# Kernel tuning notes

Measured on AMD Instinct MI355X. Metric: run time of the kernel, lower is better.

Reference implementation:

```python
import jax, jax.numpy as jnp
import numpy as np

L, I, H = 4, 256, 512          # layers, input_size, hidden_size
SH, LH, GH = 4, 2, 2            # short/long/global heads
NH, HD, FF = SH + LH + GH, H // (SH + LH + GH), 2 * H
S, B = 1024, 8                  # seq (AST nodes), batch
EPS = 1e-5
NEG = -1e9


def _ln(x, g, b):
    m = jnp.mean(x, axis=-1, keepdims=True)
    v = jnp.var(x, axis=-1, keepdims=True)
    return (x - m) * jax.lax.rsqrt(v + EPS) * g + b


def setup_inputs() -> dict:
    key = jax.random.key(0)
    ks = jax.random.split(key, 10)
    w = lambda k, shape: jax.random.normal(k, shape, jnp.float32) * 0.02
    return {
        "nodes": jax.random.normal(ks[0], (S, B, I), jnp.float32),
        "dist": jax.random.randint(ks[1], (B, S, S), 0, 5, jnp.int32),
        "dense_w": w(ks[2], (H, I)), "dense_b": jnp.zeros((H,), jnp.float32),
        "dense_ln_g": jnp.ones((H,), jnp.float32), "dense_ln_b": jnp.zeros((H,), jnp.float32),
        "qkv_w": w(ks[3], (L, 3 * H, H)), "qkv_b": jnp.zeros((L, 3 * H), jnp.float32),
        "out_w": w(ks[4], (L, H, H)), "out_b": jnp.zeros((L, H), jnp.float32),
        "ln1_g": jnp.ones((L, H), jnp.float32), "ln1_b": jnp.zeros((L, H), jnp.float32),
        "ffn_w1": w(ks[5], (L, FF, H)), "ffn_b1": jnp.zeros((L, FF), jnp.float32),
        "ffn_w2": w(ks[6], (L, H, FF)), "ffn_b2": jnp.zeros((L, H), jnp.float32),
        "ln2_g": jnp.ones((L, H), jnp.float32), "ln2_b": jnp.zeros((L, H), jnp.float32),
        "bn_g": jnp.ones((H,), jnp.float32), "bn_b": jnp.zeros((H,), jnp.float32),
    }


def _mask_bias(dist):
    # dist: [B,S,S] int -> additive bias [B,NH,S,S]
    short = (dist == 1)[:, None]                       # [B,1,S,S]
    longm = (dist >= 1)[:, None]
    globm = jnp.broadcast_to((dist[:, 0:1, :] >= 1)[:, None], (dist.shape[0], 1, S, S))
    allowed = jnp.concatenate([
        jnp.broadcast_to(short, (dist.shape[0], SH, S, S)),
        jnp.broadcast_to(longm, (dist.shape[0], LH, S, S)),
        jnp.broadcast_to(globm, (dist.shape[0], GH, S, S)),
    ], axis=1)
    allowed = allowed | jnp.eye(S, dtype=bool)
    return jnp.where(allowed, 0.0, NEG).astype(jnp.float32)


def _forward(nodes, dist, dense_w, dense_b, dense_ln_g, dense_ln_b,
             qkv_w, qkv_b, out_w, out_b, ln1_g, ln1_b,
             ffn_w1, ffn_b1, ffn_w2, ffn_b2, ln2_g, ln2_b, bn_g, bn_b):
    x = jnp.transpose(nodes, (1, 0, 2))                # [B,S,I]
    x = _ln(x @ dense_w.T + dense_b, dense_ln_g, dense_ln_b)  # [B,S,H]
    bias = _mask_bias(dist)                            # [B,NH,S,S]
    scale = 1.0 / np.sqrt(HD)

    def layer(x, p):
        (wqkv, bqkv, wo, bo, g1, b1, w1, bf1, w2, bf2, g2, b2) = p
        qkv = x @ wqkv.T + bqkv                        # [B,S,3H]
        q, k, v = jnp.split(qkv, 3, axis=-1)
        q = q.reshape(B, S, NH, HD).transpose(0, 2, 1, 3)
        k = k.reshape(B, S, NH, HD).transpose(0, 2, 1, 3)
        v = v.reshape(B, S, NH, HD).transpose(0, 2, 1, 3)
        scores = jnp.einsum('bhqd,bhkd->bhqk', q, k) * scale + bias
        attn = jax.nn.softmax(scores, axis=-1)
        o = jnp.einsum('bhqk,bhkd->bhqd', attn, v)
        o = o.transpose(0, 2, 1, 3).reshape(B, S, H) @ wo.T + bo
        x = _ln(x + o, g1, b1)
        f = jax.nn.relu(x @ w1.T + bf1) @ w2.T + bf2
        x = _ln(x + f, g2, b2)
        return x, None

    params = (qkv_w, qkv_b, out_w, out_b, ln1_g, ln1_b,
              ffn_w1, ffn_b1, ffn_w2, ffn_b2, ln2_g, ln2_b)
    x, _ = jax.lax.scan(layer, x, params)
    hidden = x[:, 0]                                   # first token -> [B,H]
    m = jnp.mean(hidden, axis=0)
    v = jnp.var(hidden, axis=0)
    return (hidden - m) * jax.lax.rsqrt(v + EPS) * bn_g + bn_b


def reference(nodes, dist, dense_w, dense_b, dense_ln_g, dense_ln_b,
              qkv_w, qkv_b, out_w, out_b, ln1_g, ln1_b,
              ffn_w1, ffn_b1, ffn_w2, ffn_b2, ln2_g, ln2_b, bn_g, bn_b):
    return _forward(nodes, dist, dense_w, dense_b, dense_ln_g, dense_ln_b,
                    qkv_w, qkv_b, out_w, out_b, ln1_g, ln1_b,
                    ffn_w1, ffn_b1, ffn_w2, ffn_b2, ln2_g, ln2_b, bn_g, bn_b)
```

## Files before the change

kernel.cpp:

```cpp
#include <hip/hip_runtime.h>
#include <hip/hip_bf16.h>
#include <math.h>

#define LAYERS 4
#define IDIM 256
#define HDIM 512
#define NH 8
#define HD 64
#define FF 1024
#define SEQ 1024
#define BATCH 8
#define EPS 1e-5f

typedef __attribute__((ext_vector_type(8))) short short8;
typedef __attribute__((ext_vector_type(4))) short short4v;
typedef __attribute__((ext_vector_type(4))) float f32x4;
typedef __attribute__((ext_vector_type(4))) int int4v;
typedef __attribute__((ext_vector_type(2))) unsigned int uint2v;
typedef unsigned long long u64;

__device__ __forceinline__ short f2bf(float f) {
    unsigned u = __float_as_uint(f);
    u = (u + 0x7FFFu + ((u >> 16) & 1u)) >> 16;
    return (short)u;
}
__device__ __forceinline__ float bf2f(short s) {
    return __uint_as_float(((unsigned)(unsigned short)s) << 16);
}
__device__ __forceinline__ void gll16(const void* g, void* l) {
    __builtin_amdgcn_global_load_lds(
        (const __attribute__((address_space(1))) unsigned int*)g,
        (__attribute__((address_space(3))) unsigned int*)l, 16, 0, 0);
}

#define CVT_P0 131072u
#define CVT_P1 3276800u
#define CVT_P2 4325376u
#define CVT_P3 6422528u
#define CVT_TOT 8519680u
__global__ __launch_bounds__(256) void cvt_all(const float* __restrict__ s0, short* __restrict__ d0,
                                               const float* __restrict__ s1, short* __restrict__ d1,
                                               const float* __restrict__ s2, short* __restrict__ d2,
                                               const float* __restrict__ s3, short* __restrict__ d3,
                                               const float* __restrict__ s4, short* __restrict__ d4) {
    size_t i = ((size_t)blockIdx.x * 256 + threadIdx.x) * 4;
    const float* s; short* d; size_t off;
    if (i < CVT_P0)      { s = s0; d = d0; off = i; }
    else if (i < CVT_P1) { s = s1; d = d1; off = i - CVT_P0; }
    else if (i < CVT_P2) { s = s2; d = d2; off = i - CVT_P1; }
    else if (i < CVT_P3) { s = s3; d = d3; off = i - CVT_P2; }
    else                 { s = s4; d = d4; off = i - CVT_P3; }
    f32x4 f = *(const f32x4*)(s + off);
    short4v o = {f2bf(f[0]), f2bf(f[1]), f2bf(f[2]), f2bf(f[3])};
    *(short4v*)(d + off) = o;
}

__global__ __launch_bounds__(256) void transpose_nodes(const float* __restrict__ nodes,
                                                       short* __restrict__ xt) {
    size_t idx = ((size_t)blockIdx.x * 256 + threadIdx.x) * 4;
    int i  = idx & (IDIM - 1);
    int sb = idx >> 8;
    int b  = sb & (BATCH - 1);
    int s  = sb >> 3;
    f32x4 f = *(const f32x4*)(nodes + idx);
    short4v o = {f2bf(f[0]), f2bf(f[1]), f2bf(f[2]), f2bf(f[3])};
    *(short4v*)(xt + ((size_t)b * SEQ + s) * IDIM + i) = o;
}

__global__ __launch_bounds__(256) void build_masks(const int* __restrict__ dist,
                                                   u64* __restrict__ mS,
                                                   u64* __restrict__ mL,
                                                   u64* __restrict__ mG) {
    int t = blockIdx.x * 256 + threadIdx.x;
    int w = t & 15, q = (t >> 4) & 1023, b = t >> 14;
    const int4v* dp = (const int4v*)(dist + ((size_t)b * SEQ + q) * SEQ + w * 64);
    u64 bs = 0, bl = 0;
#pragma unroll
    for (int i = 0; i < 16; i++) {
        int4v d = dp[i];
#pragma unroll
        for (int j = 0; j < 4; j++) {
            bs |= (u64)(d[j] == 1) << (i * 4 + j);
            bl |= (u64)(d[j] >= 1) << (i * 4 + j);
        }
    }
    mS[((size_t)b * SEQ + q) * 16 + w] = bs;
    mL[((size_t)b * SEQ + q) * 16 + w] = bl;
    if (q == 0) mG[b * 16 + w] = bl;
}

template<int BM, int BK>
__global__ __launch_bounds__(256, 2)
void gemm_bf16(const short* __restrict__ A, const short* __restrict__ W,
               const float* __restrict__ bias, short* __restrict__ C,
               short* __restrict__ vt, int M, int N, int K, int relu) {
    constexpr int UPR = BK / 8;
    constexpr int RPC = 512 / BK;
    __shared__ __align__(16) short As[BM * BK];
    __shared__ __align__(16) short Ws[128 * BK];
    const int tid = threadIdx.x;
    const int w = tid >> 6, lane = tid & 63;
    const int l15 = lane & 15, quad = lane >> 4;
    const int m0 = blockIdx.y * BM, n0 = blockIdx.x * 128;

    constexpr int NI = (BM == 128) ? 4 : 2;
    const int wm = (BM == 128) ? (w >> 1) * 64 : 0;
    const int wn = (BM == 128) ? (w & 1) * 64 : w * 32;

    f32x4 acc[4][NI];
#pragma unroll
    for (int mi = 0; mi < 4; mi++)
#pragma unroll
        for (int ni = 0; ni < NI; ni++) acc[mi][ni] = (f32x4){0.f, 0.f, 0.f, 0.f};

    const int r_in = (BK == 64) ? (lane >> 3) : (lane >> 4);
    const int c8   = lane & (UPR - 1);

    for (int k0 = 0; k0 < K; k0 += BK) {
#pragma unroll
        for (int rep = 0; rep < BM * BK / 2048; rep++) {
            int chunk = rep * 4 + w;
            int row = chunk * RPC + r_in;
            const short* src = A + (size_t)(m0 + row) * K + k0 + ((c8 ^ (row & (UPR - 1))) << 3);
            gll16(src, (char*)As + chunk * 1024);
        }
#pragma unroll
        for (int rep = 0; rep < 128 * BK / 2048; rep++) {
            int chunk = rep * 4 + w;
            int row = chunk * RPC + r_in;
            const short* src = W + (size_t)(n0 + row) * K + k0 + ((c8 ^ (row & (UPR - 1))) << 3);
            gll16(src, (char*)Ws + chunk * 1024);
        }
        __syncthreads();
#pragma unroll
        for (int ks = 0; ks < BK / 32; ks++) {
            short8 af[4], wf[NI];
            const int dblk = ks * 4 + quad;
#pragma unroll
            for (int mi = 0; mi < 4; mi++) {
                int row = wm + mi * 16 + l15;
                af[mi] = *(const short8*)((const char*)As + row * (BK * 2) + ((dblk ^ (row & (UPR - 1))) << 4));
            }
#pragma unroll
            for (int ni = 0; ni < NI; ni++) {
                int row = wn + ni * 16 + l15;
                wf[ni] = *(const short8*)((const char*)Ws + row * (BK * 2) + ((dblk ^ (row & (UPR - 1))) << 4));
            }
#pragma unroll
            for (int mi = 0; mi < 4; mi++)
#pragma unroll
                for (int ni = 0; ni < NI; ni++)
                    acc[mi][ni] = __builtin_amdgcn_mfma_f32_16x16x32_bf16(
                        af[mi], wf[ni], acc[mi][ni], 0, 0, 0);
        }
        __syncthreads();
    }
    if (vt && n0 >= 1024) {
#pragma unroll
        for (int ni = 0; ni < NI; ni++) {
            int n = n0 + wn + ni * 16 + l15;
            int d = n - 1024, h = d >> 6, dd = d & 63;
            float bz = bias[n];
#pragma unroll
            for (int mi = 0; mi < 4; mi++) {
                int mbase = m0 + wm + mi * 16 + quad * 4;
                int b = mbase >> 10, s = mbase & 1023;
                int tile = s >> 6, j = (s & 63) >> 2;
                size_t off = ((size_t)(b * NH + h) * HD + dd) * SEQ
                           + tile * 64 + (j & 7) * 8 + (j >> 3) * 4;
                short4v pk;
#pragma unroll
                for (int r = 0; r < 4; r++) pk[r] = f2bf(acc[mi][ni][r] + bz);
                *(short4v*)(vt + off) = pk;
            }
        }
    } else {
#pragma unroll
        for (int ni = 0; ni < NI; ni++) {
            int n = n0 + wn + ni * 16 + l15;
            float bz = bias[n];
#pragma unroll
            for (int mi = 0; mi < 4; mi++) {
#pragma unroll
                for (int r = 0; r < 4; r++) {
                    int m = m0 + wm + mi * 16 + quad * 4 + r;
                    float v = acc[mi][ni][r] + bz;
                    if (relu) v = fmaxf(v, 0.f);
                    C[(size_t)m * N + n] = f2bf(v);
                }
            }
        }
    }
}

#define EXP2SC 0.18033688011112042f
__global__ __launch_bounds__(256, 4)
void attn_mfma(const short* __restrict__ qkv, const short* __restrict__ vt,
               const u64* __restrict__ maskS, const u64* __restrict__ maskL,
               const u64* __restrict__ maskG, short* __restrict__ out) {
    const int tid = threadIdx.x;
    const int w = tid >> 6, lane = tid & 63, l15 = lane & 15, quad = lane >> 4;
    const int p = blockIdx.x;
    const int g_ = (p & 7) + 8 * (p >> 7);
    const int qt = (p >> 3) & 15;
    const int b = g_ >> 3, h = g_ & 7;
    const int q = qt * 64 + w * 16 + l15;

    __shared__ __align__(16) short Ks[128 * 64];
    __shared__ __align__(16) short Vs[128 * 64];

    short8 qf[2];
    {
        const short* qrow = qkv + ((size_t)(b * SEQ + q) * 1536) + h * 64;
#pragma unroll
        for (int ks = 0; ks < 2; ks++)
            qf[ks] = *(const short8*)(qrow + ks * 32 + quad * 8);
    }
    const u64* mrow = (h < 4) ? (maskS + ((size_t)b * SEQ + q) * 16)
                   : (h < 6) ? (maskL + ((size_t)b * SEQ + q) * 16)
                   :           (maskG + (size_t)b * 16);

    f32x4 of[4];
#pragma unroll
    for (int mt = 0; mt < 4; mt++) of[mt] = (f32x4){0.f, 0.f, 0.f, 0.f};
    float lsum = 0.f;

    const int r_in = lane >> 3, c8 = lane & 7;
    const int swz = (c8 ^ r_in) << 3;
    const short* kp = qkv + ((size_t)b * SEQ + r_in) * 1536 + 512 + h * 64 + swz;
    const short* vp = vt + ((size_t)((b * NH + h) * HD) + r_in) * SEQ + swz;
    const int fsw = (l15 & 7);

    for (int kt = 0; kt < SEQ; kt += 128) {
#pragma unroll
        for (int rep = 0; rep < 4; rep++) {
            int c = rep * 4 + w;
            gll16(kp + (size_t)(kt + c * 8) * 1536, (char*)Ks + c * 1024);
        }
#pragma unroll
        for (int rep = 0; rep < 4; rep++) {
            int v = rep * 4 + w;
            gll16(vp + (size_t)((v & 7) * 8) * SEQ + kt + (v >> 3) * 64,
                  (char*)Vs + v * 1024);
        }
        __syncthreads();

#pragma unroll
        for (int t = 0; t < 2; t++) {
            f32x4 sa[4];
#pragma unroll
            for (int g = 0; g < 4; g++) sa[g] = (f32x4){0.f, 0.f, 0.f, 0.f};
#pragma unroll
            for (int ks = 0; ks < 2; ks++) {
                const int dblk = ks * 4 + quad;
#pragma unroll
                for (int g = 0; g < 4; g++) {
                    int row = t * 64 + g * 16 + l15;
                    short8 kf = *(const short8*)((const char*)Ks + row * 128 + ((dblk ^ fsw) << 4));
                    sa[g] = __builtin_amdgcn_mfma_f32_16x16x32_bf16(kf, qf[ks], sa[g], 0, 0, 0);
                }
            }
            u64 mw = mrow[(kt >> 6) + t];
            if ((q >> 6) == (kt >> 6) + t) mw |= 1ull << (q & 63);
            u64 mq = mw >> (quad * 4);
            unsigned mlo = (unsigned)mq, mhi = (unsigned)(mq >> 32);
            short4v pfrag[4];
#pragma unroll
            for (int g = 0; g < 4; g++) {
                unsigned mg = ((g & 2) ? mhi : mlo) >> ((g & 1) * 16);
                float pv[4];
#pragma unroll
                for (int r = 0; r < 4; r++) {
                    float bias = ((mg >> r) & 1u) ? 0.f : -1e9f;
                    pv[r] = exp2f(fmaf(sa[g][r], EXP2SC, bias));
                    lsum += pv[r];
                }
                uint2v pk;
                pk[0] = __builtin_amdgcn_perm(__float_as_uint(pv[1]), __float_as_uint(pv[0]), 0x07060302u);
                pk[1] = __builtin_amdgcn_perm(__float_as_uint(pv[3]), __float_as_uint(pv[2]), 0x07060302u);
                pfrag[g] = __builtin_bit_cast(short4v, pk);
            }
#pragma unroll
            for (int g01 = 0; g01 < 2; g01++) {
                const int u = g01 * 4 + quad;
#pragma unroll
                for (int mt = 0; mt < 4; mt++) {
                    int row = mt * 16 + l15;
                    short8 vv = *(const short8*)((const char*)Vs + t * 8192 + row * 128 + ((u ^ fsw) << 4));
                    short4v vlo = {vv[0], vv[1], vv[2], vv[3]};
                    short4v vhi = {vv[4], vv[5], vv[6], vv[7]};
                    of[mt] = __builtin_amdgcn_mfma_f32_16x16x16bf16_1k(vlo, pfrag[g01], of[mt], 0, 0, 0);
                    of[mt] = __builtin_amdgcn_mfma_f32_16x16x16bf16_1k(vhi, pfrag[g01 + 2], of[mt], 0, 0, 0);
                }
            }
        }
        __syncthreads();
    }
    lsum += __shfl_xor(lsum, 16);
    lsum += __shfl_xor(lsum, 32);
    float inv = 1.f / lsum;
#pragma unroll
    for (int mt = 0; mt < 4; mt++) {
        short4v pk;
#pragma unroll
        for (int r = 0; r < 4; r++) pk[r] = f2bf(of[mt][r] * inv);
        *(short4v*)(out + ((size_t)(b * SEQ + q) * HDIM) + h * 64 + mt * 16 + quad * 4) = pk;
    }
}

__global__ __launch_bounds__(256) void ln_bf16(const short* __restrict__ x,
                                               const short* __restrict__ r,
                                               const float* __restrict__ g,
                                               const float* __restrict__ b,
                                               short* __restrict__ y) {
    const int wv = threadIdx.x >> 6, lane = threadIdx.x & 63;
    const size_t row = (size_t)blockIdx.x * 4 + wv;
    const size_t base = row * HDIM + lane * 8;
    short8 xv = *(const short8*)(x + base);
    float v[8];
#pragma unroll
    for (int i = 0; i < 8; i++) v[i] = bf2f(xv[i]);
    if (r) {
        short8 rv = *(const short8*)(r + base);
#pragma unroll
        for (int i = 0; i < 8; i++) v[i] += bf2f(rv[i]);
    }
    float s = 0.f, ss = 0.f;
#pragma unroll
    for (int i = 0; i < 8; i++) { s += v[i]; ss += v[i] * v[i]; }
#pragma unroll
    for (int off = 1; off < 64; off <<= 1) {
        s  += __shfl_xor(s, off);
        ss += __shfl_xor(ss, off);
    }
    const float mean = s * (1.f / HDIM);
    const float var  = ss * (1.f / HDIM) - mean * mean;
    const float inv  = rsqrtf(var + EPS);
    f32x4 g0 = *(const f32x4*)(g + lane * 8), g1 = *(const f32x4*)(g + lane * 8 + 4);
    f32x4 b0 = *(const f32x4*)(b + lane * 8), b1 = *(const f32x4*)(b + lane * 8 + 4);
    short8 o;
#pragma unroll
    for (int i = 0; i < 4; i++) o[i]     = f2bf((v[i]     - mean) * inv * g0[i] + b0[i]);
#pragma unroll
    for (int i = 0; i < 4; i++) o[i + 4] = f2bf((v[i + 4] - mean) * inv * g1[i] + b1[i]);
    *(short8*)(y + base) = o;
}

__global__ __launch_bounds__(256) void final_bn(const short* __restrict__ X,
                                                const float* __restrict__ g,
                                                const float* __restrict__ bb,
                                                float* __restrict__ out) {
    int h = blockIdx.x * 256 + threadIdx.x;
    if (h >= HDIM) return;
    float vals[BATCH];
    float m = 0.f;
#pragma unroll
    for (int b = 0; b < BATCH; b++) {
        vals[b] = bf2f(X[(size_t)b * SEQ * HDIM + h]);
        m += vals[b];
    }
    m *= (1.f / BATCH);
    float v = 0.f;
#pragma unroll
    for (int b = 0; b < BATCH; b++) { float d = vals[b] - m; v += d * d; }
    v *= (1.f / BATCH);
    float inv = rsqrtf(v + EPS);
#pragma unroll
    for (int b = 0; b < BATCH; b++)
        out[b * HDIM + h] = (vals[b] - m) * inv * g[h] + bb[h];
}

extern "C" void kernel_launch(void* const* d_in, const int* in_sizes, int n_in,
                              void* d_out, int out_size, void* d_ws, size_t ws_size,
                              hipStream_t stream) {
    const float* nodes      = (const float*)d_in[0];
    const int*   dist       = (const int*)  d_in[1];
    const float* dense_w    = (const float*)d_in[2];
    const float* dense_b    = (const float*)d_in[3];
    const float* dense_ln_g = (const float*)d_in[4];
    const float* dense_ln_b = (const float*)d_in[5];
    const float* qkv_w      = (const float*)d_in[6];
    const float* qkv_b      = (const float*)d_in[7];
    const float* out_w      = (const float*)d_in[8];
    const float* out_b      = (const float*)d_in[9];
    const float* ln1_g      = (const float*)d_in[10];
    const float* ln1_b      = (const float*)d_in[11];
    const float* ffn_w1     = (const float*)d_in[12];
    const float* ffn_b1     = (const float*)d_in[13];
    const float* ffn_w2     = (const float*)d_in[14];
    const float* ffn_b2     = (const float*)d_in[15];
    const float* ln2_g      = (const float*)d_in[16];
    const float* ln2_b      = (const float*)d_in[17];
    const float* bn_g       = (const float*)d_in[18];
    const float* bn_b       = (const float*)d_in[19];
    float* out = (float*)d_out;

    const int M = BATCH * SEQ;
    const size_t MB = 1024 * 1024;
    char* ws = (char*)d_ws;
    short* Wd   = (short*)(ws + 0 * MB);
    short* Wqkv = (short*)(ws + 1 * MB);
    short* Wo   = (short*)(ws + 9 * MB);
    short* W1   = (short*)(ws + 13 * MB);
    short* W2   = (short*)(ws + 18 * MB);
    u64*   mS   = (u64*)(ws + 23 * MB);
    u64*   mL   = (u64*)(ws + 24 * MB);
    u64*   mG   = (u64*)(ws + 25 * MB);
    short* X    = (short*)(ws + 26 * MB);
    short* QKV  = (short*)(ws + 34 * MB);
    short* Vt   = (short*)(ws + 58 * MB);
    short* AT   = (short*)(ws + 66 * MB);
    short* O2   = (short*)(ws + 74 * MB);
    short* XT   = QKV;
    short* F1   = QKV;
    short* F2   = AT;

    cvt_all<<<CVT_TOT / 1024, 256, 0, stream>>>(dense_w, Wd, qkv_w, Wqkv,
                                                out_w, Wo, ffn_w1, W1, ffn_w2, W2);
    transpose_nodes<<<(SEQ * BATCH * IDIM) / 1024, 256, 0, stream>>>(nodes, XT);
    build_masks<<<(BATCH * SEQ * 16) / 256, 256, 0, stream>>>(dist, mS, mL, mG);

    gemm_bf16<64, 128><<<dim3(HDIM / 128, M / 64), 256, 0, stream>>>(
        XT, Wd, dense_b, O2, nullptr, M, HDIM, IDIM, 0);
    ln_bf16<<<M / 4, 256, 0, stream>>>(O2, nullptr, dense_ln_g, dense_ln_b, X);

    for (int l = 0; l < LAYERS; l++) {
        const short* wqkv = Wqkv + (size_t)l * 3 * HDIM * HDIM;
        const float* bqkv = qkv_b + (size_t)l * 3 * HDIM;
        const short* wo   = Wo + (size_t)l * HDIM * HDIM;
        const float* bo   = out_b + (size_t)l * HDIM;
        const short* w1   = W1 + (size_t)l * FF * HDIM;
        const float* b1   = ffn_b1 + (size_t)l * FF;
        const short* w2   = W2 + (size_t)l * HDIM * FF;
        const float* b2   = ffn_b2 + (size_t)l * HDIM;

        gemm_bf16<128, 64><<<dim3(3 * HDIM / 128, M / 128), 256, 0, stream>>>(
            X, wqkv, bqkv, QKV, Vt, M, 3 * HDIM, HDIM, 0);
        attn_mfma<<<1024, 256, 0, stream>>>(QKV, Vt, mS, mL, mG, AT);
        gemm_bf16<64, 128><<<dim3(HDIM / 128, M / 64), 256, 0, stream>>>(
            AT, wo, bo, O2, nullptr, M, HDIM, HDIM, 0);
        ln_bf16<<<M / 4, 256, 0, stream>>>(X, O2, ln1_g + l * HDIM, ln1_b + l * HDIM, X);
        gemm_bf16<128, 64><<<dim3(FF / 128, M / 128), 256, 0, stream>>>(
            X, w1, b1, F1, nullptr, M, FF, HDIM, 1);
        gemm_bf16<64, 128><<<dim3(HDIM / 128, M / 64), 256, 0, stream>>>(
            F1, w2, b2, F2, nullptr, M, HDIM, FF, 0);
        ln_bf16<<<M / 4, 256, 0, stream>>>(X, F2, ln2_g + l * HDIM, ln2_b + l * HDIM, X);
    }
    final_bn<<<(HDIM + 255) / 256, 256, 0, stream>>>(X, bn_g, bn_b, out);
}
```

Measured before the change: 643.3 us.

## Double-buffer GEMM shared-memory tiles and switch all GEMMs to 64x64 tiles

Adds ping-pong LDS buffers to the bf16 GEMM so the next K-slab's async global-to-LDS loads are issued before computing the current slab, dropping one barrier per iteration. All GEMM launches switch to BM=64, BK=64 tiles, which gives more blocks for the M=8192 problem, and launch bounds are raised to 3 blocks per CU. The change trades smaller per-block reuse for more parallelism and load/compute overlap, and the doubled LDS and tighter register budget may limit occupancy.

```diff
diff --git a/kernel.cpp b/kernel.cpp
--- a/kernel.cpp
+++ b/kernel.cpp
@@ -90,14 +90,16 @@
 }
 
 template<int BM, int BK>
-__global__ __launch_bounds__(256, 2)
+__global__ __launch_bounds__(256, 3)
 void gemm_bf16(const short* __restrict__ A, const short* __restrict__ W,
                const float* __restrict__ bias, short* __restrict__ C,
                short* __restrict__ vt, int M, int N, int K, int relu) {
     constexpr int UPR = BK / 8;
-    constexpr int RPC = 512 / BK;
-    __shared__ __align__(16) short As[BM * BK];
-    __shared__ __align__(16) short Ws[128 * BK];
+    constexpr int RPC = 1024 / (BK * 2);
+    constexpr int ACH = BM * BK * 2 / 1024;
+    constexpr int WCH = 128 * BK * 2 / 1024;
+    __shared__ __align__(16) short As[2][BM * BK];
+    __shared__ __align__(16) short Ws[2][128 * BK];
     const int tid = threadIdx.x;
     const int w = tid >> 6, lane = tid & 63;
     const int l15 = lane & 15, quad = lane >> 4;
@@ -113,25 +115,33 @@
 #pragma unroll
         for (int ni = 0; ni < NI; ni++) acc[mi][ni] = (f32x4){0.f, 0.f, 0.f, 0.f};
 
-    const int r_in = (BK == 64) ? (lane >> 3) : (lane >> 4);
-    const int c8   = lane & (UPR - 1);
-
-    for (int k0 = 0; k0 < K; k0 += BK) {
-#pragma unroll
-        for (int rep = 0; rep < BM * BK / 2048; rep++) {
+    const int r_in = lane / UPR;
+    const int c8   = lane % UPR;
+
+    auto stage = [&](int buf, int k0) {
+#pragma unroll
+        for (int rep = 0; rep < ACH / 4; rep++) {
             int chunk = rep * 4 + w;
             int row = chunk * RPC + r_in;
-            const short* src = A + (size_t)(m0 + row) * K + k0 + ((c8 ^ (row & (UPR - 1))) << 3);
-            gll16(src, (char*)As + chunk * 1024);
-        }
-#pragma unroll
-        for (int rep = 0; rep < 128 * BK / 2048; rep++) {
+            gll16(A + (size_t)(m0 + row) * K + k0 + ((c8 ^ (row & (UPR - 1))) << 3),
+                  (char*)As[buf] + chunk * 1024);
+        }
+#pragma unroll
+        for (int rep = 0; rep < WCH / 4; rep++) {
             int chunk = rep * 4 + w;
             int row = chunk * RPC + r_in;
-            const short* src = W + (size_t)(n0 + row) * K + k0 + ((c8 ^ (row & (UPR - 1))) << 3);
-            gll16(src, (char*)Ws + chunk * 1024);
-        }
+            gll16(W + (size_t)(n0 + row) * K + k0 + ((c8 ^ (row & (UPR - 1))) << 3),
+                  (char*)Ws[buf] + chunk * 1024);
+        }
+    };
+
+    stage(0, 0);
+    const int NIT = K / BK;
+    for (int it = 0; it < NIT; it++) {
         __syncthreads();
+        if (it + 1 < NIT) stage((it + 1) & 1, (it + 1) * BK);
+        const char* Ab = (const char*)As[it & 1];
+        const char* Wb = (const char*)Ws[it & 1];
 #pragma unroll
         for (int ks = 0; ks < BK / 32; ks++) {
             short8 af[4], wf[NI];
@@ -139,12 +149,12 @@
 #pragma unroll
             for (int mi = 0; mi < 4; mi++) {
                 int row = wm + mi * 16 + l15;
-                af[mi] = *(const short8*)((const char*)As + row * (BK * 2) + ((dblk ^ (row & (UPR - 1))) << 4));
+                af[mi] = *(const short8*)(Ab + row * (BK * 2) + ((dblk ^ (row & (UPR - 1))) << 4));
             }
 #pragma unroll
             for (int ni = 0; ni < NI; ni++) {
                 int row = wn + ni * 16 + l15;
-                wf[ni] = *(const short8*)((const char*)Ws + row * (BK * 2) + ((dblk ^ (row & (UPR - 1))) << 4));
+                wf[ni] = *(const short8*)(Wb + row * (BK * 2) + ((dblk ^ (row & (UPR - 1))) << 4));
             }
 #pragma unroll
             for (int mi = 0; mi < 4; mi++)
@@ -153,7 +163,6 @@
                     acc[mi][ni] = __builtin_amdgcn_mfma_f32_16x16x32_bf16(
                         af[mi], wf[ni], acc[mi][ni], 0, 0, 0);
         }
-        __syncthreads();
     }
     if (vt && n0 >= 1024) {
 #pragma unroll
@@ -420,7 +429,7 @@
     transpose_nodes<<<(SEQ * BATCH * IDIM) / 1024, 256, 0, stream>>>(nodes, XT);
     build_masks<<<(BATCH * SEQ * 16) / 256, 256, 0, stream>>>(dist, mS, mL, mG);
 
-    gemm_bf16<64, 128><<<dim3(HDIM / 128, M / 64), 256, 0, stream>>>(
+    gemm_bf16<64, 64><<<dim3(HDIM / 128, M / 64), 256, 0, stream>>>(
         XT, Wd, dense_b, O2, nullptr, M, HDIM, IDIM, 0);
     ln_bf16<<<M / 4, 256, 0, stream>>>(O2, nullptr, dense_ln_g, dense_ln_b, X);
 
@@ -434,15 +443,15 @@
         const short* w2   = W2 + (size_t)l * HDIM * FF;
         const float* b2   = ffn_b2 + (size_t)l * HDIM;
 
-        gemm_bf16<128, 64><<<dim3(3 * HDIM / 128, M / 128), 256, 0, stream>>>(
+        gemm_bf16<64, 64><<<dim3(3 * HDIM / 128, M / 64), 256, 0, stream>>>(
             X, wqkv, bqkv, QKV, Vt, M, 3 * HDIM, HDIM, 0);
         attn_mfma<<<1024, 256, 0, stream>>>(QKV, Vt, mS, mL, mG, AT);
-        gemm_bf16<64, 128><<<dim3(HDIM / 128, M / 64), 256, 0, stream>>>(
+        gemm_bf16<64, 64><<<dim3(HDIM / 128, M / 64), 256, 0, stream>>>(
             AT, wo, bo, O2, nullptr, M, HDIM, HDIM, 0);
         ln_bf16<<<M / 4, 256, 0, stream>>>(X, O2, ln1_g + l * HDIM, ln1_b + l * HDIM, X);
-        gemm_bf16<128, 64><<<dim3(FF / 128, M / 128), 256, 0, stream>>>(
+        gemm_bf16<64, 64><<<dim3(FF / 128, M / 64), 256, 0, stream>>>(
             X, w1, b1, F1, nullptr, M, FF, HDIM, 1);
-        gemm_bf16<64, 128><<<dim3(HDIM / 128, M / 64), 256, 0, stream>>>(
+        gemm_bf16<64, 64><<<dim3(HDIM / 128, M / 64), 256, 0, stream>>>(
             F1, w2, b2, F2, nullptr, M, HDIM, FF, 0);
         ln_bf16<<<M / 4, 256, 0, stream>>>(X, F2, ln2_g + l * HDIM, ln2_b + l * HDIM, X);
     }
```

Result: no change. 654.7 us (+1.8%).

## Use 16x16x32 MFMA for PV, permute K rows, fuse prep kernels

Applied to the files above, without the earlier changes.

Merges the three preprocessing kernels (weight conversion, node transpose, mask build) into one launch to cut launch overhead. In attention, the K tile is loaded with a permuted row order so that each lane's score fragment lines up with a contiguous 8-key chunk. That lets P·V use a single 16x16x32 bf16 MFMA per V read instead of two 16x16x16 ops, and V is now written in plain key order. The mask is applied by zeroing exp values instead of adding a -1e9 bias, using the hardware exp2 builtin. The row sum is split into two accumulators. The scheme relies on the K permutation, mask bit shifts and V layout staying consistent.

```diff
diff --git a/kernel.cpp b/kernel.cpp
--- a/kernel.cpp
+++ b/kernel.cpp
@@ -16,7 +16,7 @@
 typedef __attribute__((ext_vector_type(4))) short short4v;
 typedef __attribute__((ext_vector_type(4))) float f32x4;
 typedef __attribute__((ext_vector_type(4))) int int4v;
-typedef __attribute__((ext_vector_type(2))) unsigned int uint2v;
+typedef __attribute__((ext_vector_type(4))) unsigned int uint4v;
 typedef unsigned long long u64;
 
 __device__ __forceinline__ short f2bf(float f) {
@@ -31,6 +31,13 @@
     __builtin_amdgcn_global_load_lds(
         (const __attribute__((address_space(1))) unsigned int*)g,
         (__attribute__((address_space(3))) unsigned int*)l, 16, 0, 0);
+}
+__device__ __forceinline__ float fexp2(float x) {
+#if __has_builtin(__builtin_amdgcn_exp2f)
+    return __builtin_amdgcn_exp2f(x);
+#else
+    return exp2f(x);
+#endif
 }
 
 #define CVT_P0 131072u
@@ -38,55 +45,54 @@
 #define CVT_P2 4325376u
 #define CVT_P3 6422528u
 #define CVT_TOT 8519680u
-__global__ __launch_bounds__(256) void cvt_all(const float* __restrict__ s0, short* __restrict__ d0,
-                                               const float* __restrict__ s1, short* __restrict__ d1,
-                                               const float* __restrict__ s2, short* __restrict__ d2,
-                                               const float* __restrict__ s3, short* __restrict__ d3,
-                                               const float* __restrict__ s4, short* __restrict__ d4) {
-    size_t i = ((size_t)blockIdx.x * 256 + threadIdx.x) * 4;
-    const float* s; short* d; size_t off;
-    if (i < CVT_P0)      { s = s0; d = d0; off = i; }
-    else if (i < CVT_P1) { s = s1; d = d1; off = i - CVT_P0; }
-    else if (i < CVT_P2) { s = s2; d = d2; off = i - CVT_P1; }
-    else if (i < CVT_P3) { s = s3; d = d3; off = i - CVT_P2; }
-    else                 { s = s4; d = d4; off = i - CVT_P3; }
-    f32x4 f = *(const f32x4*)(s + off);
-    short4v o = {f2bf(f[0]), f2bf(f[1]), f2bf(f[2]), f2bf(f[3])};
-    *(short4v*)(d + off) = o;
-}
-
-__global__ __launch_bounds__(256) void transpose_nodes(const float* __restrict__ nodes,
-                                                       short* __restrict__ xt) {
-    size_t idx = ((size_t)blockIdx.x * 256 + threadIdx.x) * 4;
-    int i  = idx & (IDIM - 1);
-    int sb = idx >> 8;
-    int b  = sb & (BATCH - 1);
-    int s  = sb >> 3;
-    f32x4 f = *(const f32x4*)(nodes + idx);
-    short4v o = {f2bf(f[0]), f2bf(f[1]), f2bf(f[2]), f2bf(f[3])};
-    *(short4v*)(xt + ((size_t)b * SEQ + s) * IDIM + i) = o;
-}
-
-__global__ __launch_bounds__(256) void build_masks(const int* __restrict__ dist,
-                                                   u64* __restrict__ mS,
-                                                   u64* __restrict__ mL,
-                                                   u64* __restrict__ mG) {
-    int t = blockIdx.x * 256 + threadIdx.x;
-    int w = t & 15, q = (t >> 4) & 1023, b = t >> 14;
-    const int4v* dp = (const int4v*)(dist + ((size_t)b * SEQ + q) * SEQ + w * 64);
-    u64 bs = 0, bl = 0;
-#pragma unroll
-    for (int i = 0; i < 16; i++) {
-        int4v d = dp[i];
-#pragma unroll
-        for (int j = 0; j < 4; j++) {
-            bs |= (u64)(d[j] == 1) << (i * 4 + j);
-            bl |= (u64)(d[j] >= 1) << (i * 4 + j);
-        }
-    }
-    mS[((size_t)b * SEQ + q) * 16 + w] = bs;
-    mL[((size_t)b * SEQ + q) * 16 + w] = bl;
-    if (q == 0) mG[b * 16 + w] = bl;
+__global__ __launch_bounds__(256) void prep_all(
+    const float* __restrict__ s0, short* __restrict__ d0,
+    const float* __restrict__ s1, short* __restrict__ d1,
+    const float* __restrict__ s2, short* __restrict__ d2,
+    const float* __restrict__ s3, short* __restrict__ d3,
+    const float* __restrict__ s4, short* __restrict__ d4,
+    const float* __restrict__ nodes, short* __restrict__ xt,
+    const int* __restrict__ dist, u64* __restrict__ mS,
+    u64* __restrict__ mL, u64* __restrict__ mG) {
+    int blk = blockIdx.x;
+    if (blk < 8320) {
+        size_t i = ((size_t)blk * 256 + threadIdx.x) * 4;
+        const float* s; short* d; size_t off;
+        if (i < CVT_P0)      { s = s0; d = d0; off = i; }
+        else if (i < CVT_P1) { s = s1; d = d1; off = i - CVT_P0; }
+        else if (i < CVT_P2) { s = s2; d = d2; off = i - CVT_P1; }
+        else if (i < CVT_P3) { s = s3; d = d3; off = i - CVT_P2; }
+        else                 { s = s4; d = d4; off = i - CVT_P3; }
+        f32x4 f = *(const f32x4*)(s + off);
+        short4v o = {f2bf(f[0]), f2bf(f[1]), f2bf(f[2]), f2bf(f[3])};
+        *(short4v*)(d + off) = o;
+    } else if (blk < 8320 + 2048) {
+        size_t idx = ((size_t)(blk - 8320) * 256 + threadIdx.x) * 4;
+        int i  = idx & (IDIM - 1);
+        int sb = idx >> 8;
+        int b  = sb & (BATCH - 1);
+        int s  = sb >> 3;
+        f32x4 f = *(const f32x4*)(nodes + idx);
+        short4v o = {f2bf(f[0]), f2bf(f[1]), f2bf(f[2]), f2bf(f[3])};
+        *(short4v*)(xt + ((size_t)b * SEQ + s) * IDIM + i) = o;
+    } else {
+        int t = (blk - 10368) * 256 + threadIdx.x;
+        int w = t & 15, q = (t >> 4) & 1023, b = t >> 14;
+        const int4v* dp = (const int4v*)(dist + ((size_t)b * SEQ + q) * SEQ + w * 64);
+        u64 bs = 0, bl = 0;
+#pragma unroll
+        for (int i = 0; i < 16; i++) {
+            int4v d = dp[i];
+#pragma unroll
+            for (int j = 0; j < 4; j++) {
+                bs |= (u64)(d[j] == 1) << (i * 4 + j);
+                bl |= (u64)(d[j] >= 1) << (i * 4 + j);
+            }
+        }
+        mS[((size_t)b * SEQ + q) * 16 + w] = bs;
+        mL[((size_t)b * SEQ + q) * 16 + w] = bl;
+        if (q == 0) mG[b * 16 + w] = bl;
+    }
 }
 
 template<int BM, int BK>
@@ -165,9 +171,7 @@
             for (int mi = 0; mi < 4; mi++) {
                 int mbase = m0 + wm + mi * 16 + quad * 4;
                 int b = mbase >> 10, s = mbase & 1023;
-                int tile = s >> 6, j = (s & 63) >> 2;
-                size_t off = ((size_t)(b * NH + h) * HD + dd) * SEQ
-                           + tile * 64 + (j & 7) * 8 + (j >> 3) * 4;
+                size_t off = ((size_t)(b * NH + h) * HD + dd) * SEQ + s;
                 short4v pk;
 #pragma unroll
                 for (int r = 0; r < 4; r++) pk[r] = f2bf(acc[mi][ni][r] + bz);
@@ -223,11 +227,11 @@
     f32x4 of[4];
 #pragma unroll
     for (int mt = 0; mt < 4; mt++) of[mt] = (f32x4){0.f, 0.f, 0.f, 0.f};
-    float lsum = 0.f;
+    float ls0 = 0.f, ls1 = 0.f;
 
     const int r_in = lane >> 3, c8 = lane & 7;
     const int swz = (c8 ^ r_in) << 3;
-    const short* kp = qkv + ((size_t)b * SEQ + r_in) * 1536 + 512 + h * 64 + swz;
+    const short* kbase = qkv + ((size_t)b * SEQ) * 1536 + 512 + h * 64 + swz;
     const short* vp = vt + ((size_t)((b * NH + h) * HD) + r_in) * SEQ + swz;
     const int fsw = (l15 & 7);
 
@@ -235,7 +239,11 @@
 #pragma unroll
         for (int rep = 0; rep < 4; rep++) {
             int c = rep * 4 + w;
-            gll16(kp + (size_t)(kt + c * 8) * 1536, (char*)Ks + c * 1024);
+            int pr = c * 8 + r_in;
+            int pt = pr & 63;
+            int key = (pr & 64) | (pt & 32) | (((pt >> 2) & 3) << 3)
+                    | (((pt >> 4) & 1) << 2) | (pt & 3);
+            gll16(kbase + (size_t)(kt + key) * 1536, (char*)Ks + c * 1024);
         }
 #pragma unroll
         for (int rep = 0; rep < 4; rep++) {
@@ -262,40 +270,48 @@
             }
             u64 mw = mrow[(kt >> 6) + t];
             if ((q >> 6) == (kt >> 6) + t) mw |= 1ull << (q & 63);
-            u64 mq = mw >> (quad * 4);
-            unsigned mlo = (unsigned)mq, mhi = (unsigned)(mq >> 32);
-            short4v pfrag[4];
+            u64 mq2 = mw >> (quad * 8);
+            unsigned mlo = (unsigned)mq2, mhi = (unsigned)(mq2 >> 32);
+            float pv[4][4];
 #pragma unroll
             for (int g = 0; g < 4; g++) {
-                unsigned mg = ((g & 2) ? mhi : mlo) >> ((g & 1) * 16);
-                float pv[4];
+                unsigned mg = ((g & 2) ? mhi : mlo) >> ((g & 1) * 4);
 #pragma unroll
                 for (int r = 0; r < 4; r++) {
-                    float bias = ((mg >> r) & 1u) ? 0.f : -1e9f;
-                    pv[r] = exp2f(fmaf(sa[g][r], EXP2SC, bias));
-                    lsum += pv[r];
+                    float e = fexp2(sa[g][r] * EXP2SC);
+                    e = ((mg >> r) & 1u) ? e : 0.f;
+                    pv[g][r] = e;
+                    if (g & 1) ls1 += e; else ls0 += e;
                 }
-                uint2v pk;
-                pk[0] = __builtin_amdgcn_perm(__float_as_uint(pv[1]), __float_as_uint(pv[0]), 0x07060302u);
-                pk[1] = __builtin_amdgcn_perm(__float_as_uint(pv[3]), __float_as_uint(pv[2]), 0x07060302u);
-                pfrag[g] = __builtin_bit_cast(short4v, pk);
-            }
-#pragma unroll
-            for (int g01 = 0; g01 < 2; g01++) {
-                const int u = g01 * 4 + quad;
+            }
+            short8 pfrag[2];
+#pragma unroll
+            for (int g32 = 0; g32 < 2; g32++) {
+                uint4v pk;
+                pk[0] = __builtin_amdgcn_perm(__float_as_uint(pv[2 * g32][1]),
+                                              __float_as_uint(pv[2 * g32][0]), 0x07060302u);
+                pk[1] = __builtin_amdgcn_perm(__float_as_uint(pv[2 * g32][3]),
+                                              __float_as_uint(pv[2 * g32][2]), 0x07060302u);
+                pk[2] = __builtin_amdgcn_perm(__float_as_uint(pv[2 * g32 + 1][1]),
+                                              __float_as_uint(pv[2 * g32 + 1][0]), 0x07060302u);
+                pk[3] = __builtin_amdgcn_perm(__float_as_uint(pv[2 * g32 + 1][3]),
+                                              __float_as_uint(pv[2 * g32 + 1][2]), 0x07060302u);
+                pfrag[g32] = __builtin_bit_cast(short8, pk);
+            }
+#pragma unroll
+            for (int g32 = 0; g32 < 2; g32++) {
+                const int u = g32 * 4 + quad;
 #pragma unroll
                 for (int mt = 0; mt < 4; mt++) {
                     int row = mt * 16 + l15;
-                    short8 vv = *(const short8*)((const char*)Vs + t * 8192 + row * 128 + ((u ^ fsw) << 4));
-                    short4v vlo = {vv[0], vv[1], vv[2], vv[3]};
-                    short4v vhi = {vv[4], vv[5], vv[6], vv[7]};
-                    of[mt] = __builtin_amdgcn_mfma_f32_16x16x16bf16_1k(vlo, pfrag[g01], of[mt], 0, 0, 0);
-                    of[mt] = __builtin_amdgcn_mfma_f32_16x16x16bf16_1k(vhi, pfrag[g01 + 2], of[mt], 0, 0, 0);
+                    short8 vf = *(const short8*)((const char*)Vs + t * 8192 + row * 128 + ((u ^ fsw) << 4));
+                    of[mt] = __builtin_amdgcn_mfma_f32_16x16x32_bf16(vf, pfrag[g32], of[mt], 0, 0, 0);
                 }
             }
         }
         __syncthreads();
     }
+    float lsum = ls0 + ls1;
     lsum += __shfl_xor(lsum, 16);
     lsum += __shfl_xor(lsum, 32);
     float inv = 1.f / lsum;
@@ -415,10 +431,9 @@
     short* F1   = QKV;
     short* F2   = AT;
 
-    cvt_all<<<CVT_TOT / 1024, 256, 0, stream>>>(dense_w, Wd, qkv_w, Wqkv,
-                                                out_w, Wo, ffn_w1, W1, ffn_w2, W2);
-    transpose_nodes<<<(SEQ * BATCH * IDIM) / 1024, 256, 0, stream>>>(nodes, XT);
-    build_masks<<<(BATCH * SEQ * 16) / 256, 256, 0, stream>>>(dist, mS, mL, mG);
+    prep_all<<<10880, 256, 0, stream>>>(dense_w, Wd, qkv_w, Wqkv, out_w, Wo,
+                                        ffn_w1, W1, ffn_w2, W2,
+                                        nodes, XT, dist, mS, mL, mG);
 
     gemm_bf16<64, 128><<<dim3(HDIM / 128, M / 64), 256, 0, stream>>>(
         XT, Wd, dense_b, O2, nullptr, M, HDIM, IDIM, 0);
```

After: 610.6 us. 5.1% less time.
